# Kernel optimization log

Measured on AMD Instinct MI355X. Metric: run time of the kernel, lower is better.

## Reference

```python
import jax, jax.numpy as jnp
import numpy as np

T, H, E = 1024, 2048, 32
I = 1024            # moe_intermediate_size
K = 8               # num_experts_per_token
G = 4               # num_expert_group
TOPK_GROUP = 2
N_SHARED = 2
IS = I * N_SHARED   # shared-expert intermediate
RSF = 2.5           # routed_scaling_factor


def setup_inputs() -> dict:
    key = jax.random.key(0)
    ks = jax.random.split(key, 9)
    s = 0.02
    return {
        "hidden_states": jax.random.normal(ks[0], (T, H), jnp.float32),
        "gate_w": jax.random.normal(ks[1], (H, E), jnp.float32) * s,
        "corr_bias": jax.random.normal(ks[2], (E,), jnp.float32) * s,
        "w_gate": jax.random.normal(ks[3], (E, H, I), jnp.float32) * s,
        "w_up": jax.random.normal(ks[4], (E, H, I), jnp.float32) * s,
        "w_down": jax.random.normal(ks[5], (E, I, H), jnp.float32) * s,
        "sw_gate": jax.random.normal(ks[6], (H, IS), jnp.float32) * s,
        "sw_up": jax.random.normal(ks[7], (H, IS), jnp.float32) * s,
        "sw_down": jax.random.normal(ks[8], (IS, H), jnp.float32) * s,
    }


def _route(x, gate_w, corr_bias):
    # biased grouped top-k (DeepSeek-V3 style sigmoid routing)
    logits = x @ gate_w                      # [T,E]
    scores = jax.nn.sigmoid(logits)
    sfc = scores + corr_bias[None, :]        # scores for choice
    grp = sfc.reshape(-1, G, E // G)
    # group score = sum of top-2 biased scores within the group
    grp_score = jax.lax.top_k(grp, 2)[0].sum(-1)          # [T,G]
    _, gidx = jax.lax.top_k(grp_score, TOPK_GROUP)        # [T,topk_group]
    rows = jnp.arange(sfc.shape[0])[:, None]
    gmask = jnp.zeros((sfc.shape[0], G), sfc.dtype).at[rows, gidx].set(1.0)
    emask = jnp.repeat(gmask, E // G, axis=1)             # [T,E]
    masked = jnp.where(emask > 0, sfc, -jnp.inf)
    _, idx = jax.lax.top_k(masked, K)                     # [T,K]
    w = jnp.take_along_axis(scores, idx, axis=1)          # unbiased scores
    w = w / w.sum(-1, keepdims=True)                      # renormalize
    w = w * RSF                                           # routed scaling
    combine = jnp.zeros((sfc.shape[0], E), x.dtype).at[rows, idx].add(w)
    return combine                                        # dense [T,E] combine weights


def reference(hidden_states, gate_w, corr_bias, w_gate, w_up, w_down,
              sw_gate, sw_up, sw_down):
    x = hidden_states
    # shared experts (SiLU-gated MLP)
    shared = (jax.nn.silu(x @ sw_gate) * (x @ sw_up)) @ sw_down   # [T,H]
    # routing
    combine = _route(x, gate_w, corr_bias)                        # [T,E]
    # routed experts (dense grouped-GEMM reference)
    g = jnp.einsum('th,ehi->tei', x, w_gate)
    u = jnp.einsum('th,ehi->tei', x, w_up)
    a = jax.nn.silu(g) * u                                        # [T,E,I]
    y = jnp.einsum('tei,eih->teh', a, w_down)                     # [T,E,H]
    routed = jnp.einsum('teh,te->th', y, combine)
    return routed + shared
```

## Files before the change

### kernel.cpp

```cpp
#include <hip/hip_runtime.h>

#define T_TOK 1024
#define H_DIM 2048
#define E_NUM 32
#define I_DIM 1024
#define IS_DIM 2048

typedef float  f32x4 __attribute__((ext_vector_type(4)));
typedef short  s16x8 __attribute__((ext_vector_type(8)));
typedef unsigned short u16x4 __attribute__((ext_vector_type(4)));
typedef unsigned short u16x8 __attribute__((ext_vector_type(8)));

__device__ __forceinline__ unsigned short f2bf(float f) {
    unsigned u = __builtin_bit_cast(unsigned, f);
    u = (u + 0x7fffu + ((u >> 16) & 1u)) >> 16;
    return (unsigned short)u;
}

__device__ __forceinline__ int swz(int r, int c) {
    return (r << 5) + (c ^ (((r >> 2) & 3) << 3));
}

__global__ __launch_bounds__(256) void route_k(
    const float* __restrict__ x, const float* __restrict__ gw,
    const float* __restrict__ bias, int* __restrict__ tidx,
    float* __restrict__ tw)
{
    const int w = threadIdx.x >> 6;
    const int lane = threadIdx.x & 63;
    const int t = blockIdx.x * 4 + w;
    __shared__ float xs[4][H_DIM];
    __shared__ float sfc[4][E_NUM];
    __shared__ float sc[4][E_NUM];

    for (int i = threadIdx.x; i < 4 * (H_DIM / 4); i += 256) {
        int tt = i >> 9;
        int c = i & 511;
        *(f32x4*)&xs[tt][c * 4] =
            *(const f32x4*)(x + (size_t)(blockIdx.x * 4 + tt) * H_DIM + c * 4);
    }
    __syncthreads();

    const int eq = (lane & 7) * 4;
    const int hs = lane >> 3;
    f32x4 acc = {0.f, 0.f, 0.f, 0.f};
    #pragma unroll 4
    for (int h = hs; h < H_DIM; h += 8) {
        float xv = xs[w][h];
        f32x4 gv = *(const f32x4*)(gw + (size_t)h * E_NUM + eq);
        acc += gv * xv;
    }
    #pragma unroll
    for (int m = 8; m < 64; m <<= 1) {
        acc[0] += __shfl_xor(acc[0], m);
        acc[1] += __shfl_xor(acc[1], m);
        acc[2] += __shfl_xor(acc[2], m);
        acc[3] += __shfl_xor(acc[3], m);
    }
    if (lane < 8) {
        #pragma unroll
        for (int j = 0; j < 4; ++j) {
            float s = 1.f / (1.f + expf(-acc[j]));
            sc[w][eq + j] = s;
            sfc[w][eq + j] = s + bias[eq + j];
        }
    }
    __syncthreads();

    if (lane == 0) {
        float gs[4];
        for (int gg = 0; gg < 4; ++gg) {
            float m1 = -1e30f, m2 = -1e30f;
            for (int j = 0; j < 8; ++j) {
                float v = sfc[w][gg * 8 + j];
                if (v > m1) { m2 = m1; m1 = v; }
                else if (v > m2) { m2 = v; }
            }
            gs[gg] = m1 + m2;
        }
        int g1 = 0;
        for (int gg = 1; gg < 4; ++gg) if (gs[gg] > gs[g1]) g1 = gg;
        int g2 = (g1 == 0) ? 1 : 0;
        for (int gg = 0; gg < 4; ++gg)
            if (gg != g1 && gs[gg] > gs[g2]) g2 = gg;

        unsigned allow = (0xFFu << (g1 * 8)) | (0xFFu << (g2 * 8));
        unsigned taken = 0u;
        int   isel[8];
        float wsel[8];
        float wsum = 0.f;
        for (int k = 0; k < 8; ++k) {
            int best = 0; float bv = -1e30f;
            for (int e2 = 0; e2 < 32; ++e2) {
                if (((allow >> e2) & 1u) && !((taken >> e2) & 1u)) {
                    float v = sfc[w][e2];
                    if (v > bv) { bv = v; best = e2; }
                }
            }
            taken |= 1u << best;
            isel[k] = best;
            wsel[k] = sc[w][best];
            wsum += sc[w][best];
        }
        const float f = 2.5f / wsum;
        for (int k = 0; k < 8; ++k) {
            tidx[t * 8 + k] = isel[k];
            tw[t * 8 + k] = wsel[k] * f;
        }
    }
}

__global__ __launch_bounds__(64) void build_k(
    const int* __restrict__ tidx, const float* __restrict__ tw,
    int* __restrict__ ltok, float* __restrict__ lw, int* __restrict__ counts)
{
    const int e = blockIdx.x;
    const int lane = threadIdx.x;
    int cnt = 0;
    for (int t0 = 0; t0 < T_TOK; t0 += 64) {
        const int t = t0 + lane;
        int sel = 0; float w = 0.f;
        #pragma unroll
        for (int k = 0; k < 8; ++k) {
            if (tidx[t * 8 + k] == e) { sel = 1; w = tw[t * 8 + k]; }
        }
        unsigned long long m = __ballot(sel);
        int pos = __popcll(m & ((1ull << lane) - 1ull));
        if (sel) {
            ltok[e * T_TOK + cnt + pos] = t;
            lw[e * T_TOK + cnt + pos] = w;
        }
        cnt += __popcll(m);
    }
    if (lane == 0) counts[e] = cnt;
}

__global__ void prefix_k(const int* __restrict__ counts, int* __restrict__ offsets)
{
    if (threadIdx.x == 0) {
        int off = 0;
        for (int e = 0; e < E_NUM; ++e) { offsets[e] = off; off += counts[e]; }
    }
}

template<int DUAL, int EXPERT, int ABF16, int ATOMIC, int BM>
__global__ __launch_bounds__(512) void gemm_k(
    const void* __restrict__ Av, const float* __restrict__ B1g,
    const float* __restrict__ B2g, void* __restrict__ outv,
    const int* __restrict__ counts, const int* __restrict__ offsets,
    const int* __restrict__ ltok, const float* __restrict__ lw,
    int M, int N, int K)
{
    constexpr int FM  = BM / 64;
    constexpr int WR  = BM / 4;
    constexpr int TPR = 512 / BM;
    constexpr int KSP = 32 / TPR;
    constexpr int NL  = KSP / 4;
    constexpr int NB  = KSP / 8;

    const int e = blockIdx.z;
    const int Mloc = EXPERT ? counts[e] : M;
    const int col0 = blockIdx.y * 64;
    const int rb = EXPERT ? offsets[e] : 0;

    const float* B1 = B1g;
    const float* B2 = B2g;
    if (EXPERT) {
        size_t eo = (size_t)e * K * N;
        B1 += eo;
        if (DUAL) B2 += eo;
    }

    __shared__ unsigned short lA[2][BM * 32];
    __shared__ unsigned short lB[2][DUAL + 1][64 * 32];

    const int tid = threadIdx.x;
    const int lane = tid & 63;
    const int wv = tid >> 6;
    const int wm = wv >> 1;
    const int wn = wv & 1;

    const int arow = tid / TPR;
    const int akb  = (tid % TPR) * KSP;

    const bool doB = tid < (DUAL ? 256 : 128);
    const int bmat = DUAL ? (tid >> 7) : 0;
    const int t7 = tid & 127;
    const int nq = t7 & 15;
    const int kq = t7 >> 4;
    const float* bp = (bmat ? B2 : B1) + (size_t)(4 * kq) * N + col0 + nq * 4;

    f32x4 acc1[FM][2], acc2[FM][2];
    f32x4 paX[NL], paY[NL];
    u16x8 pbaX[NB], pbaY[NB];
    f32x4 pbX[4], pbY[4];

    const float* apf = nullptr;
    const unsigned short* apb = nullptr;

    auto loadT = [&](int k0, f32x4 (&pa)[NL], u16x8 (&pba)[NB], f32x4 (&pb)[4]) {
        if (ABF16) {
            #pragma unroll
            for (int i = 0; i < NB; ++i)
                pba[i] = *(const u16x8*)(apb + k0 + i * 8);
        } else {
            #pragma unroll
            for (int i = 0; i < NL; ++i)
                pa[i] = *(const f32x4*)(apf + k0 + i * 4);
        }
        if (doB) {
            #pragma unroll
            for (int j = 0; j < 4; ++j)
                pb[j] = *(const f32x4*)(bp + (size_t)(k0 + j) * N);
        }
    };

    auto storeT = [&](int p, f32x4 (&pa)[NL], u16x8 (&pba)[NB], f32x4 (&pb)[4]) {
        if (ABF16) {
            #pragma unroll
            for (int i = 0; i < NB; ++i)
                *(u16x8*)&lA[p][swz(arow, akb + i * 8)] = pba[i];
        } else {
            #pragma unroll
            for (int i = 0; i < NL; i += 2) {
                u16x8 h = { f2bf(pa[i][0]),   f2bf(pa[i][1]),
                            f2bf(pa[i][2]),   f2bf(pa[i][3]),
                            f2bf(pa[i+1][0]), f2bf(pa[i+1][1]),
                            f2bf(pa[i+1][2]), f2bf(pa[i+1][3]) };
                *(u16x8*)&lA[p][swz(arow, akb + i * 4)] = h;
            }
        }
        if (doB) {
            #pragma unroll
            for (int j2 = 0; j2 < 4; ++j2) {
                u16x4 h = { f2bf(pb[0][j2]), f2bf(pb[1][j2]),
                            f2bf(pb[2][j2]), f2bf(pb[3][j2]) };
                *(u16x4*)&lB[p][bmat][swz(nq * 4 + j2, kq * 4)] = h;
            }
        }
    };

    auto compute = [&](int p) {
        const int koff = (lane >> 4) * 8;
        s16x8 af[FM], b1f[2], b2f[2];
        #pragma unroll
        for (int fm = 0; fm < FM; ++fm)
            af[fm] = *(const s16x8*)&lA[p][swz(wm * WR + fm * 16 + (lane & 15), koff)];
        #pragma unroll
        for (int fn = 0; fn < 2; ++fn) {
            b1f[fn] = *(const s16x8*)&lB[p][0][swz(wn * 32 + fn * 16 + (lane & 15), koff)];
            if (DUAL)
                b2f[fn] = *(const s16x8*)&lB[p][1][swz(wn * 32 + fn * 16 + (lane & 15), koff)];
        }
        #pragma unroll
        for (int fm = 0; fm < FM; ++fm)
            #pragma unroll
            for (int fn = 0; fn < 2; ++fn) {
                acc1[fm][fn] = __builtin_amdgcn_mfma_f32_16x16x32_bf16(
                    af[fm], b1f[fn], acc1[fm][fn], 0, 0, 0);
                if (DUAL)
                    acc2[fm][fn] = __builtin_amdgcn_mfma_f32_16x16x32_bf16(
                        af[fm], b2f[fn], acc2[fm][fn], 0, 0, 0);
            }
    };

    const int nk = K >> 5;

    for (int row0 = blockIdx.x * BM; row0 < Mloc; row0 += gridDim.x * BM) {
        {
            int rr = row0 + arow;
            if (rr >= Mloc) rr = Mloc - 1;
            if (ABF16) {
                apb = (const unsigned short*)Av + (size_t)(rb + rr) * K + akb;
            } else {
                int grow = EXPERT ? ltok[e * T_TOK + rr] : rr;
                apf = (const float*)Av + (size_t)grow * K + akb;
            }
        }
        #pragma unroll
        for (int a = 0; a < FM; ++a)
            #pragma unroll
            for (int b = 0; b < 2; ++b) {
                acc1[a][b] = f32x4{0.f, 0.f, 0.f, 0.f};
                acc2[a][b] = f32x4{0.f, 0.f, 0.f, 0.f};
            }

        loadT(0, paX, pbaX, pbX);
        loadT(32, paY, pbaY, pbY);
        __syncthreads();
        storeT(0, paX, pbaX, pbX);
        __syncthreads();

        for (int kt = 0; kt < nk; kt += 2) {
            if (kt + 2 < nk) loadT((kt + 2) << 5, paX, pbaX, pbX);
            compute(0);
            storeT(1, paY, pbaY, pbY);
            __syncthreads();
            if (kt + 3 < nk) loadT((kt + 3) << 5, paY, pbaY, pbY);
            compute(1);
            if (kt + 2 < nk) {
                storeT(0, paX, pbaX, pbX);
                __syncthreads();
            }
        }

        const int fr = (lane >> 4) << 2;
        const int fc = lane & 15;
        if (DUAL) {
            unsigned short* outp = (unsigned short*)outv;
            #pragma unroll
            for (int fm = 0; fm < FM; ++fm)
                #pragma unroll
                for (int fn = 0; fn < 2; ++fn)
                    #pragma unroll
                    for (int j = 0; j < 4; ++j) {
                        int r = wm * WR + fm * 16 + fr + j;
                        if (row0 + r < Mloc) {
                            int cc = col0 + wn * 32 + fn * 16 + fc;
                            float gv = acc1[fm][fn][j];
                            float uv = acc2[fm][fn][j];
                            float a = gv / (1.f + expf(-gv)) * uv;
                            outp[(size_t)(rb + row0 + r) * N + cc] = f2bf(a);
                        }
                    }
        } else if (ATOMIC) {
            float* outp = (float*)outv;
            #pragma unroll
            for (int fm = 0; fm < FM; ++fm)
                #pragma unroll
                for (int fn = 0; fn < 2; ++fn)
                    #pragma unroll
                    for (int j = 0; j < 4; ++j) {
                        int r = wm * WR + fm * 16 + fr + j;
                        if (row0 + r < Mloc) {
                            int tok = ltok[e * T_TOK + row0 + r];
                            float wr = lw[e * T_TOK + row0 + r];
                            int cc = col0 + wn * 32 + fn * 16 + fc;
                            atomicAdd(outp + (size_t)tok * N + cc, acc1[fm][fn][j] * wr);
                        }
                    }
        } else {
            float* outp = (float*)outv;
            #pragma unroll
            for (int fm = 0; fm < FM; ++fm)
                #pragma unroll
                for (int fn = 0; fn < 2; ++fn)
                    #pragma unroll
                    for (int j = 0; j < 4; ++j) {
                        int r = wm * WR + fm * 16 + fr + j;
                        if (row0 + r < Mloc) {
                            int cc = col0 + wn * 32 + fn * 16 + fc;
                            outp[(size_t)(row0 + r) * N + cc] = acc1[fm][fn][j];
                        }
                    }
        }
    }
}

extern "C" void kernel_launch(void* const* d_in, const int* in_sizes, int n_in,
                              void* d_out, int out_size, void* d_ws, size_t ws_size,
                              hipStream_t stream) {
    const float* x       = (const float*)d_in[0];
    const float* gate_w  = (const float*)d_in[1];
    const float* bias    = (const float*)d_in[2];
    const float* w_gate  = (const float*)d_in[3];
    const float* w_up    = (const float*)d_in[4];
    const float* w_down  = (const float*)d_in[5];
    const float* sw_gate = (const float*)d_in[6];
    const float* sw_up   = (const float*)d_in[7];
    const float* sw_down = (const float*)d_in[8];
    float* out = (float*)d_out;

    char* ws = (char*)d_ws;
    int*   topk_idx = (int*)ws;
    float* topk_w   = (float*)(ws + 32768);
    int*   counts   = (int*)(ws + 65536);
    int*   offsets  = (int*)(ws + 65536 + 128);
    int*   ltok     = (int*)(ws + 65536 + 256);
    float* lw       = (float*)(ws + 65536 + 256 + 131072);
    unsigned short* act_s = (unsigned short*)(ws + 65536 + 256 + 262144);
    unsigned short* act_r = act_s + (size_t)T_TOK * IS_DIM;

    route_k<<<T_TOK / 4, 256, 0, stream>>>(x, gate_w, bias, topk_idx, topk_w);
    build_k<<<E_NUM, 64, 0, stream>>>(topk_idx, topk_w, ltok, lw, counts);
    prefix_k<<<1, 64, 0, stream>>>(counts, offsets);

    gemm_k<1,0,0,0,128><<<dim3(8, 32, 1), 512, 0, stream>>>(
        x, sw_gate, sw_up, act_s, nullptr, nullptr, nullptr, nullptr,
        T_TOK, IS_DIM, H_DIM);
    gemm_k<1,1,0,0,256><<<dim3(1, 16, 32), 512, 0, stream>>>(
        x, w_gate, w_up, act_r, counts, offsets, ltok, lw,
        T_TOK, I_DIM, H_DIM);
    gemm_k<0,0,1,0,128><<<dim3(8, 32, 1), 512, 0, stream>>>(
        act_s, sw_down, nullptr, out, nullptr, nullptr, nullptr, nullptr,
        T_TOK, H_DIM, IS_DIM);
    gemm_k<0,1,1,1,256><<<dim3(1, 32, 32), 512, 0, stream>>>(
        act_r, w_down, nullptr, out, counts, offsets, ltok, lw,
        T_TOK, H_DIM, I_DIM);
}
```

Measured before the change: 716.0 us.

## Pre-convert activations to bf16 once and shrink GEMM blocks to 256 threads

Adds a conversion kernel that turns the fp32 hidden states into a bf16 buffer once. All GEMMs then load bf16 A tiles directly, with gathered rows for the routed gate/up GEMM, instead of loading fp32 and converting per tile in every column block. The GEMM is also restructured to 256-thread blocks with two wave rows, smaller BM tiles, more row blocks in the grid and launch bounds targeting four blocks per CU. The aim is to halve A-side traffic, remove repeated conversion work and raise occupancy, at the cost of an extra kernel launch and more workspace.

```diff
diff --git a/kernel.cpp b/kernel.cpp
--- a/kernel.cpp
+++ b/kernel.cpp
@@ -19,6 +19,17 @@
 
 __device__ __forceinline__ int swz(int r, int c) {
     return (r << 5) + (c ^ (((r >> 2) & 3) << 3));
+}
+
+__global__ __launch_bounds__(256) void cvt_k(
+    const float* __restrict__ x, unsigned short* __restrict__ xb)
+{
+    const int i = (blockIdx.x * 256 + threadIdx.x) * 8;
+    f32x4 a = *(const f32x4*)(x + i);
+    f32x4 b = *(const f32x4*)(x + i + 4);
+    u16x8 h = { f2bf(a[0]), f2bf(a[1]), f2bf(a[2]), f2bf(a[3]),
+                f2bf(b[0]), f2bf(b[1]), f2bf(b[2]), f2bf(b[3]) };
+    *(u16x8*)(xb + i) = h;
 }
 
 __global__ __launch_bounds__(256) void route_k(
@@ -143,19 +154,18 @@
     }
 }
 
-template<int DUAL, int EXPERT, int ABF16, int ATOMIC, int BM>
-__global__ __launch_bounds__(512) void gemm_k(
-    const void* __restrict__ Av, const float* __restrict__ B1g,
+template<int DUAL, int EXPERT, int GATHER, int ATOMIC, int BM>
+__global__ __launch_bounds__(256, 4) void gemm_k(
+    const unsigned short* __restrict__ A, const float* __restrict__ B1g,
     const float* __restrict__ B2g, void* __restrict__ outv,
     const int* __restrict__ counts, const int* __restrict__ offsets,
     const int* __restrict__ ltok, const float* __restrict__ lw,
     int M, int N, int K)
 {
-    constexpr int FM  = BM / 64;
-    constexpr int WR  = BM / 4;
-    constexpr int TPR = 512 / BM;
+    constexpr int WR  = BM / 2;
+    constexpr int FM  = WR / 16;
+    constexpr int TPR = 256 / BM;
     constexpr int KSP = 32 / TPR;
-    constexpr int NL  = KSP / 4;
     constexpr int NB  = KSP / 8;
 
     const int e = blockIdx.z;
@@ -191,23 +201,14 @@
     const float* bp = (bmat ? B2 : B1) + (size_t)(4 * kq) * N + col0 + nq * 4;
 
     f32x4 acc1[FM][2], acc2[FM][2];
-    f32x4 paX[NL], paY[NL];
     u16x8 pbaX[NB], pbaY[NB];
     f32x4 pbX[4], pbY[4];
-
-    const float* apf = nullptr;
     const unsigned short* apb = nullptr;
 
-    auto loadT = [&](int k0, f32x4 (&pa)[NL], u16x8 (&pba)[NB], f32x4 (&pb)[4]) {
-        if (ABF16) {
-            #pragma unroll
-            for (int i = 0; i < NB; ++i)
-                pba[i] = *(const u16x8*)(apb + k0 + i * 8);
-        } else {
-            #pragma unroll
-            for (int i = 0; i < NL; ++i)
-                pa[i] = *(const f32x4*)(apf + k0 + i * 4);
-        }
+    auto loadT = [&](int k0, u16x8 (&pba)[NB], f32x4 (&pb)[4]) {
+        #pragma unroll
+        for (int i = 0; i < NB; ++i)
+            pba[i] = *(const u16x8*)(apb + k0 + i * 8);
         if (doB) {
             #pragma unroll
             for (int j = 0; j < 4; ++j)
@@ -215,21 +216,10 @@
         }
     };
 
-    auto storeT = [&](int p, f32x4 (&pa)[NL], u16x8 (&pba)[NB], f32x4 (&pb)[4]) {
-        if (ABF16) {
-            #pragma unroll
-            for (int i = 0; i < NB; ++i)
-                *(u16x8*)&lA[p][swz(arow, akb + i * 8)] = pba[i];
-        } else {
-            #pragma unroll
-            for (int i = 0; i < NL; i += 2) {
-                u16x8 h = { f2bf(pa[i][0]),   f2bf(pa[i][1]),
-                            f2bf(pa[i][2]),   f2bf(pa[i][3]),
-                            f2bf(pa[i+1][0]), f2bf(pa[i+1][1]),
-                            f2bf(pa[i+1][2]), f2bf(pa[i+1][3]) };
-                *(u16x8*)&lA[p][swz(arow, akb + i * 4)] = h;
-            }
-        }
+    auto storeT = [&](int p, u16x8 (&pba)[NB], f32x4 (&pb)[4]) {
+        #pragma unroll
+        for (int i = 0; i < NB; ++i)
+            *(u16x8*)&lA[p][swz(arow, akb + i * 8)] = pba[i];
         if (doB) {
             #pragma unroll
             for (int j2 = 0; j2 < 4; ++j2) {
@@ -270,12 +260,8 @@
         {
             int rr = row0 + arow;
             if (rr >= Mloc) rr = Mloc - 1;
-            if (ABF16) {
-                apb = (const unsigned short*)Av + (size_t)(rb + rr) * K + akb;
-            } else {
-                int grow = EXPERT ? ltok[e * T_TOK + rr] : rr;
-                apf = (const float*)Av + (size_t)grow * K + akb;
-            }
+            int grow = GATHER ? ltok[e * T_TOK + rr] : (rb + rr);
+            apb = A + (size_t)grow * K + akb;
         }
         #pragma unroll
         for (int a = 0; a < FM; ++a)
@@ -285,21 +271,21 @@
                 acc2[a][b] = f32x4{0.f, 0.f, 0.f, 0.f};
             }
 
-        loadT(0, paX, pbaX, pbX);
-        loadT(32, paY, pbaY, pbY);
+        loadT(0, pbaX, pbX);
+        loadT(32, pbaY, pbY);
         __syncthreads();
-        storeT(0, paX, pbaX, pbX);
+        storeT(0, pbaX, pbX);
         __syncthreads();
 
         for (int kt = 0; kt < nk; kt += 2) {
-            if (kt + 2 < nk) loadT((kt + 2) << 5, paX, pbaX, pbX);
+            if (kt + 2 < nk) loadT((kt + 2) << 5, pbaX, pbX);
             compute(0);
-            storeT(1, paY, pbaY, pbY);
+            storeT(1, pbaY, pbY);
             __syncthreads();
-            if (kt + 3 < nk) loadT((kt + 3) << 5, paY, pbaY, pbY);
+            if (kt + 3 < nk) loadT((kt + 3) << 5, pbaY, pbY);
             compute(1);
             if (kt + 2 < nk) {
-                storeT(0, paX, pbaX, pbX);
+                storeT(0, pbaX, pbX);
                 __syncthreads();
             }
         }
@@ -380,21 +366,23 @@
     float* lw       = (float*)(ws + 65536 + 256 + 131072);
     unsigned short* act_s = (unsigned short*)(ws + 65536 + 256 + 262144);
     unsigned short* act_r = act_s + (size_t)T_TOK * IS_DIM;
-
+    unsigned short* xbf   = act_r + (size_t)T_TOK * 8 * I_DIM;
+
+    cvt_k<<<T_TOK * H_DIM / 2048, 256, 0, stream>>>(x, xbf);
     route_k<<<T_TOK / 4, 256, 0, stream>>>(x, gate_w, bias, topk_idx, topk_w);
     build_k<<<E_NUM, 64, 0, stream>>>(topk_idx, topk_w, ltok, lw, counts);
     prefix_k<<<1, 64, 0, stream>>>(counts, offsets);
 
-    gemm_k<1,0,0,0,128><<<dim3(8, 32, 1), 512, 0, stream>>>(
-        x, sw_gate, sw_up, act_s, nullptr, nullptr, nullptr, nullptr,
+    gemm_k<1,0,0,0,64><<<dim3(16, 32, 1), 256, 0, stream>>>(
+        xbf, sw_gate, sw_up, act_s, nullptr, nullptr, nullptr, nullptr,
         T_TOK, IS_DIM, H_DIM);
-    gemm_k<1,1,0,0,256><<<dim3(1, 16, 32), 512, 0, stream>>>(
-        x, w_gate, w_up, act_r, counts, offsets, ltok, lw,
+    gemm_k<1,1,1,0,128><<<dim3(2, 16, 32), 256, 0, stream>>>(
+        xbf, w_gate, w_up, act_r, counts, offsets, ltok, lw,
         T_TOK, I_DIM, H_DIM);
-    gemm_k<0,0,1,0,128><<<dim3(8, 32, 1), 512, 0, stream>>>(
+    gemm_k<0,0,0,0,64><<<dim3(16, 32, 1), 256, 0, stream>>>(
         act_s, sw_down, nullptr, out, nullptr, nullptr, nullptr, nullptr,
         T_TOK, H_DIM, IS_DIM);
-    gemm_k<0,1,1,1,256><<<dim3(1, 32, 32), 512, 0, stream>>>(
+    gemm_k<0,1,0,1,128><<<dim3(2, 32, 32), 256, 0, stream>>>(
         act_r, w_down, nullptr, out, counts, offsets, ltok, lw,
         T_TOK, H_DIM, I_DIM);
 }
```

New measurement: 855.7 us. 19.5% more time.
